# Performance work log

Hardware: AMD Instinct MI355X
Metric: run time of the kernel (lower is better)

## Reference

```python
import jax, jax.numpy as jnp
import numpy as np

B, N, D_IN = 8, 2048, 512
H = 1024          # MLP hidden
D_EMB = 512       # embed output dim
D_ATTN = 256      # attn_layers[-1]; KQ MLP outputs 2*D_ATTN


def setup_inputs() -> dict:
    key = jax.random.key(0)
    ks = jax.random.split(key, 9)
    s = lambda fi, fo: (2.0 / (fi + fo)) ** 0.5
    return {
        "x": jax.random.normal(ks[0], (B, N, D_IN), dtype=jnp.float32),
        # embed MLP: Linear(D_IN,H), ReLU, Linear(H,D_EMB)  (weights stored [in,out])
        "We1": jax.random.normal(ks[1], (D_IN, H), dtype=jnp.float32) * s(D_IN, H),
        "be1": jnp.zeros((H,), dtype=jnp.float32),
        "We2": jax.random.normal(ks[2], (H, D_EMB), dtype=jnp.float32) * s(H, D_EMB),
        "be2": jnp.zeros((D_EMB,), dtype=jnp.float32),
        # KQ MLP: Linear(D_IN,H), ReLU, Linear(H, 2*D_ATTN)
        "Wk1": jax.random.normal(ks[3], (D_IN, H), dtype=jnp.float32) * s(D_IN, H),
        "bk1": jnp.zeros((H,), dtype=jnp.float32),
        "Wk2": jax.random.normal(ks[4], (H, 2 * D_ATTN), dtype=jnp.float32) * s(H, 2 * D_ATTN),
        "bk2": jnp.zeros((2 * D_ATTN,), dtype=jnp.float32),
    }


def reference(x, We1, be1, We2, be2, Wk1, bk1, Wk2, bk2):
    # embed MLP
    embs = jax.nn.relu(x @ We1 + be1) @ We2 + be2            # [B,N,D_EMB]
    # KQ MLP; chunk: first half K, second half Q
    kq = jax.nn.relu(x @ Wk1 + bk1) @ Wk2 + bk2              # [B,N,2*D_ATTN]
    K, Q = kq[..., :D_ATTN], kq[..., D_ATTN:]
    # unscaled attention: softmax(Q K^T) V
    scores = jnp.einsum("bqd,bkd->bqk", Q, K)                # [B,N,N]
    A = jax.nn.softmax(scores, axis=-1)
    return jnp.einsum("bqk,bkd->bqd", A, embs)               # [B,N,D_EMB]
```

## Files before the change

kernel.cpp:

```cpp
#include <hip/hip_runtime.h>
#include <stdint.h>

using fx4   = __attribute__((ext_vector_type(4))) float;
using half8 = __attribute__((ext_vector_type(8))) _Float16;

__device__ __forceinline__ ushort f2h(float x) {
  _Float16 h = (_Float16)x;
  union { _Float16 hv; ushort u; } v; v.hv = h;
  return v.u;
}

__device__ __forceinline__ void gload_lds16(const ushort* g, ushort* l) {
  __builtin_amdgcn_global_load_lds(
      (__attribute__((address_space(1))) const void*)g,
      (__attribute__((address_space(3))) void*)l, 16, 0, 0);
}

#define MFMA16(a, b, c) __builtin_amdgcn_mfma_f32_16x16x32_f16(a, b, c, 0, 0, 0)

__device__ __forceinline__ void gemm_body(
    const ushort* __restrict__ A, int lda,
    const ushort* __restrict__ B, int ldb,
    const float* __restrict__ bias,
    void* __restrict__ C, int ldc,
    int K, int flags, int bx, int by,
    ushort* As, ushort* Bs)
{
  const int tid  = threadIdx.x;
  const int lane = tid & 63;
  const int wave = tid >> 6;
  const int wm   = (wave >> 1) * 64;
  const int wn   = (wave & 1) * 64;
  const long long bm = (long long)by * 128;
  const long long bn = (long long)bx * 128;

  const int srow = tid >> 2;
  const int skq  = (tid & 3) * 8;
  const ushort* a0 = A + (bm + srow) * lda + skq;
  const ushort* a1 = a0 + 64LL * lda;
  const ushort* b0 = B + (bn + srow) * ldb + skq;
  const ushort* b1 = b0 + 64LL * ldb;
  ushort* lA0 = &As[tid * 8];
  ushort* lA1 = &As[2048 + tid * 8];
  ushort* lB0 = &Bs[tid * 8];
  ushort* lB1 = &Bs[2048 + tid * 8];

  fx4 acc[4][4] = {};
  const ushort* ap = &As[(wm + (lane & 15)) * 32 + (lane >> 4) * 8];
  const ushort* bp = &Bs[(wn + (lane & 15)) * 32 + (lane >> 4) * 8];

  for (int k0 = 0; k0 < K; k0 += 32) {
    gload_lds16(a0, lA0);
    gload_lds16(a1, lA1);
    gload_lds16(b0, lB0);
    gload_lds16(b1, lB1);
    a0 += 32; a1 += 32; b0 += 32; b1 += 32;
    __syncthreads();
    half8 af[4], bv[4];
#pragma unroll
    for (int t = 0; t < 4; ++t) {
      af[t] = *(const half8*)(ap + t * 16 * 32);
      bv[t] = *(const half8*)(bp + t * 16 * 32);
    }
#pragma unroll
    for (int i = 0; i < 4; ++i)
#pragma unroll
      for (int j = 0; j < 4; ++j)
        acc[i][j] = MFMA16(af[i], bv[j], acc[i][j]);
    __syncthreads();
  }

  const int col0 = (int)bn + wn + (lane & 15);
  const int row0 = (int)bm + wm + ((lane >> 4) << 2);

  if (flags & 16) {
    ushort* Ch = (ushort*)C;
#pragma unroll
    for (int j = 0; j < 4; ++j) {
      const int col = col0 + j * 16;
      const float bvv = bias ? bias[col] : 0.0f;
#pragma unroll
      for (int i = 0; i < 4; ++i) {
        const int row = row0 + i * 16;
        ushort4 o;
        o.x = f2h(acc[i][j][0] + bvv);
        o.y = f2h(acc[i][j][1] + bvv);
        o.z = f2h(acc[i][j][2] + bvv);
        o.w = f2h(acc[i][j][3] + bvv);
        *(ushort4*)(Ch + (long long)col * ldc + row) = o;
      }
    }
    return;
  }

  float*  Cf = (float*)C;
  ushort* Ch = (ushort*)C;
#pragma unroll
  for (int j = 0; j < 4; ++j) {
    const int col = col0 + j * 16;
    const float bvv = bias ? bias[col] : 0.0f;
#pragma unroll
    for (int i = 0; i < 4; ++i) {
      const long long row = row0 + i * 16;
#pragma unroll
      for (int r = 0; r < 4; ++r) {
        float v = acc[i][j][r] + bvv;
        if (flags & 1) v = fmaxf(v, 0.0f);
        if (flags & 2) Ch[(row + r) * ldc + col] = f2h(v);
        else           Cf[(row + r) * ldc + col] = v;
      }
    }
  }
}

__global__ __launch_bounds__(256)
void gemm_bt(const ushort* __restrict__ A, int lda, long long sA,
             const ushort* __restrict__ B, int ldb, long long sB,
             const float* __restrict__ bias,
             void* __restrict__ C, int ldc, long long sC,
             int K, int flags)
{
  __shared__ ushort As[128 * 32];
  __shared__ ushort Bs[128 * 32];
  const int z = blockIdx.z;
  void* Cz = (flags & (2 | 16)) ? (void*)((ushort*)C + (long long)z * sC)
                                : (void*)((float*)C + (long long)z * sC);
  gemm_body(A + (long long)z * sA, lda, B + (long long)z * sB, ldb, bias,
            Cz, ldc, K, flags, blockIdx.x, blockIdx.y, As, Bs);
}

__global__ __launch_bounds__(256)
void gemm2_pair(const ushort* __restrict__ H, const ushort* __restrict__ W2c,
                const float* __restrict__ be2, const float* __restrict__ bk2,
                ushort* __restrict__ EMBT, ushort* __restrict__ KQ)
{
  __shared__ ushort As[128 * 32];
  __shared__ ushort Bs[128 * 32];
  if (blockIdx.z == 0)
    gemm_body(H, 2048, W2c, 1024, be2, EMBT, 16384, 1024, 16,
              blockIdx.x, blockIdx.y, As, Bs);
  else
    gemm_body(H + 1024, 2048, W2c + 524288, 1024, bk2, KQ, 512, 1024, 2,
              blockIdx.x, blockIdx.y, As, Bs);
}

__global__ __launch_bounds__(512, 2)
void attn_fused(const ushort* __restrict__ KQ, const ushort* __restrict__ EMBT,
                float* __restrict__ out)
{
  __shared__ ushort Qs[20480];
  __shared__ ushort Ps[10240];
  __shared__ float  rmax[256];
  __shared__ float  mstate[64];
  __shared__ float  mnewA[64];
  __shared__ float  alphaA[64];
  __shared__ float  lred[256];

  const int tid  = threadIdx.x;
  const int lane = tid & 63;
  const int w    = tid >> 6;
  const int c    = lane & 15;
  const int q4   = lane >> 4;
  const int qw   = w >> 2;
  const int tw   = w & 3;
  const int dw   = w * 64;
  const int z    = blockIdx.x;
  const long long tb = (long long)z * 2048;
  const int q0   = blockIdx.y * 64;

#pragma unroll
  for (int p = 0; p < 4; ++p) {
    const int cu  = p * 512 + tid;
    const int row = cu >> 5;
    const int kch = cu & 31;
    const int dc  = kch >> 2, qg = kch & 3;
    const half8 v = *(const half8*)(KQ + (tb + q0 + row) * 512 + 256 + dc * 32 + qg * 8);
    *(half8*)(Qs + dc * 2560 + row * 40 + qg * 8) = v;
  }
  if (tid < 64) mstate[tid] = -3.0e38f;
  __syncthreads();

  float l_part[2][4] = {};
  fx4 o[4][4] = {};

  for (int t0 = 0; t0 < 2048; t0 += 128) {
    half8 kb[2][8];
    const ushort* kb0 = KQ + (tb + t0 + tw * 32 + c) * 512;
    const ushort* kb1 = kb0 + 16 * 512;
#pragma unroll
    for (int dc = 0; dc < 8; ++dc) {
      kb[0][dc] = *(const half8*)(kb0 + dc * 32 + q4 * 8);
      kb[1][dc] = *(const half8*)(kb1 + dc * 32 + q4 * 8);
    }
    fx4 s[2][2] = {};
#pragma unroll
    for (int dc = 0; dc < 8; ++dc) {
      const half8 a0 = *(const half8*)(Qs + dc * 2560 + (qw * 32 + c) * 40 + q4 * 8);
      const half8 a1 = *(const half8*)(Qs + dc * 2560 + (qw * 32 + 16 + c) * 40 + q4 * 8);
      s[0][0] = MFMA16(a0, kb[0][dc], s[0][0]); s[0][1] = MFMA16(a0, kb[1][dc], s[0][1]);
      s[1][0] = MFMA16(a1, kb[0][dc], s[1][0]); s[1][1] = MFMA16(a1, kb[1][dc], s[1][1]);
    }
    half8 vb[4][4];
#pragma unroll
    for (int kc = 0; kc < 4; ++kc)
#pragma unroll
      for (int n = 0; n < 4; ++n)
        vb[kc][n] = *(const half8*)(EMBT + (long long)(dw + n * 16 + c) * 16384 +
                                    tb + t0 + kc * 32 + q4 * 8);
#pragma unroll
    for (int i = 0; i < 2; ++i) {
      fx4 rm;
#pragma unroll
      for (int r = 0; r < 4; ++r) rm[r] = fmaxf(s[i][0][r], s[i][1][r]);
#pragma unroll
      for (int off = 1; off < 16; off <<= 1)
#pragma unroll
        for (int r = 0; r < 4; ++r) rm[r] = fmaxf(rm[r], __shfl_xor(rm[r], off, 64));
      if (c == 0) {
#pragma unroll
        for (int r = 0; r < 4; ++r)
          rmax[tw * 64 + qw * 32 + i * 16 + q4 * 4 + r] = rm[r];
      }
    }
    __syncthreads();
    if (w == 0) {
      const float mo = mstate[lane];
      float mn = fmaxf(fmaxf(rmax[lane], rmax[64 + lane]),
                       fmaxf(rmax[128 + lane], rmax[192 + lane]));
      mn = fmaxf(mn, mo);
      mnewA[lane]  = mn;
      alphaA[lane] = __expf(mo - mn);
      mstate[lane] = mn;
    }
    __syncthreads();
#pragma unroll
    for (int i = 0; i < 2; ++i)
#pragma unroll
      for (int r = 0; r < 4; ++r) {
        const int q = qw * 32 + i * 16 + q4 * 4 + r;
        const float mn = mnewA[q];
        const float e0 = __expf(s[i][0][r] - mn);
        const float e1 = __expf(s[i][1][r] - mn);
        l_part[i][r] = alphaA[q] * l_part[i][r] + e0 + e1;
        Ps[tw * 2560 + q * 40 + c]      = f2h(e0);
        Ps[tw * 2560 + q * 40 + 16 + c] = f2h(e1);
      }
#pragma unroll
    for (int i4 = 0; i4 < 4; ++i4)
#pragma unroll
      for (int r = 0; r < 4; ++r) {
        const float aq = alphaA[i4 * 16 + q4 * 4 + r];
#pragma unroll
        for (int n = 0; n < 4; ++n) o[i4][n][r] *= aq;
      }
    __syncthreads();
#pragma unroll
    for (int kc = 0; kc < 4; ++kc) {
      half8 pa[4];
#pragma unroll
      for (int i4 = 0; i4 < 4; ++i4)
        pa[i4] = *(const half8*)(Ps + kc * 2560 + (i4 * 16 + c) * 40 + q4 * 8);
#pragma unroll
      for (int i4 = 0; i4 < 4; ++i4)
#pragma unroll
        for (int n = 0; n < 4; ++n)
          o[i4][n] = MFMA16(pa[i4], vb[kc][n], o[i4][n]);
    }
  }

#pragma unroll
  for (int i = 0; i < 2; ++i) {
    fx4 lv;
#pragma unroll
    for (int r = 0; r < 4; ++r) lv[r] = l_part[i][r];
#pragma unroll
    for (int off = 1; off < 16; off <<= 1)
#pragma unroll
      for (int r = 0; r < 4; ++r) lv[r] += __shfl_xor(lv[r], off, 64);
    if (c == 0) {
#pragma unroll
      for (int r = 0; r < 4; ++r)
        lred[tw * 64 + qw * 32 + i * 16 + q4 * 4 + r] = lv[r];
    }
  }
  __syncthreads();
  if (w == 0)
    alphaA[lane] = 1.0f / (lred[lane] + lred[64 + lane] + lred[128 + lane] + lred[192 + lane]);
  __syncthreads();

  float* ob = out + (tb + q0) * 512 + dw;
#pragma unroll
  for (int i4 = 0; i4 < 4; ++i4)
#pragma unroll
    for (int r = 0; r < 4; ++r) {
      const int q = i4 * 16 + q4 * 4 + r;
      const float li = alphaA[q];
#pragma unroll
      for (int n = 0; n < 4; ++n)
        ob[(long long)q * 512 + n * 16 + c] = o[i4][n][r] * li;
    }
}

__global__ __launch_bounds__(256)
void transpose_cast_w2(const float* __restrict__ in0, const float* __restrict__ in1,
                       ushort* __restrict__ out0, ushort* __restrict__ out1,
                       int R, int C) {
  __shared__ float tile[32][33];
  const float* in  = blockIdx.z ? in1 : in0;
  ushort*      outp = blockIdx.z ? out1 : out0;
  const int c0 = blockIdx.x * 32, r0 = blockIdx.y * 32;
  const int tx = threadIdx.x & 31, ty = threadIdx.x >> 5;
#pragma unroll
  for (int i = 0; i < 32; i += 8)
    tile[ty + i][tx] = in[(long long)(r0 + ty + i) * C + (c0 + tx)];
  __syncthreads();
#pragma unroll
  for (int i = 0; i < 32; i += 8)
    outp[(long long)(c0 + ty + i) * R + (r0 + tx)] = f2h(tile[tx][ty + i]);
}

__global__ __launch_bounds__(256)
void cast_f32_f16(const float* __restrict__ in, ushort* __restrict__ out) {
  const long long i = ((long long)blockIdx.x * 256 + threadIdx.x) * 4;
  const float4 v = *(const float4*)(in + i);
  ushort4 o;
  o.x = f2h(v.x); o.y = f2h(v.y); o.z = f2h(v.z); o.w = f2h(v.w);
  *(ushort4*)(out + i) = o;
}

__global__ __launch_bounds__(256)
void concat_bias(const float* __restrict__ b0, const float* __restrict__ b1,
                 float* __restrict__ out) {
  const int i = blockIdx.x * 256 + threadIdx.x;
  out[i] = (i < 1024) ? b0[i] : b1[i - 1024];
}

extern "C" void kernel_launch(void* const* d_in, const int* in_sizes, int n_in,
                              void* d_out, int out_size, void* d_ws, size_t ws_size,
                              hipStream_t stream) {
  (void)in_sizes; (void)n_in; (void)out_size; (void)ws_size;
  const float* x   = (const float*)d_in[0];
  const float* We1 = (const float*)d_in[1];
  const float* be1 = (const float*)d_in[2];
  const float* We2 = (const float*)d_in[3];
  const float* be2 = (const float*)d_in[4];
  const float* Wk1 = (const float*)d_in[5];
  const float* bk1 = (const float*)d_in[6];
  const float* Wk2 = (const float*)d_in[7];
  const float* bk2 = (const float*)d_in[8];
  float* out = (float*)d_out;
  char* ws = (char*)d_ws;

  ushort* Xb   = (ushort*)(ws + 0);
  ushort* W2c  = (ushort*)(ws + 0);
  ushort* H    = (ushort*)(ws + 16777216);
  ushort* EMBT = (ushort*)(ws + 83886080);
  ushort* KQ   = (ushort*)(ws + 100663296);
  float*  b1c  = (float*)(ws + 117440512);
  ushort* W1c  = (ushort*)(ws + 117448704);

  cast_f32_f16<<<dim3(8192), 256, 0, stream>>>(x, Xb);
  transpose_cast_w2<<<dim3(32, 16, 2), 256, 0, stream>>>(We1, Wk1, W1c, W1c + 524288, 512, 1024);
  concat_bias<<<dim3(8), 256, 0, stream>>>(be1, bk1, b1c);

  gemm_bt<<<dim3(16, 128, 1), 256, 0, stream>>>(Xb, 512, 0, W1c, 512, 0, b1c,
                                                H, 2048, 0, 512, 1 | 2);

  transpose_cast_w2<<<dim3(16, 32, 2), 256, 0, stream>>>(We2, Wk2, W2c, W2c + 524288, 1024, 512);

  gemm2_pair<<<dim3(4, 128, 2), 256, 0, stream>>>(H, W2c, be2, bk2, EMBT, KQ);

  attn_fused<<<dim3(8, 32), 512, 0, stream>>>(KQ, EMBT, out);
}
```

Baseline: 353.9 us.

## Restructure attention kernel with LDS-staged K/V tiles and per-wave softmax state

Rewrites the fused attention kernel to use 256-thread blocks covering 32 queries, loading 32-token K and V tiles into LDS via async global-to-LDS loads. Each wave keeps its own running max and sum in registers, removing the cross-wave max/sum reductions and the extra barriers of the old design. Q fragments are read directly from global each iteration instead of from LDS. The smaller query tile doubles the grid and the total K/V traffic from global, and the short key tiles add more barriers per token, with no double buffering.

```diff
diff --git a/kernel.cpp b/kernel.cpp
--- a/kernel.cpp
+++ b/kernel.cpp
@@ -144,161 +144,105 @@
               blockIdx.x, blockIdx.y, As, Bs);
 }
 
-__global__ __launch_bounds__(512, 2)
+__global__ __launch_bounds__(256, 2)
 void attn_fused(const ushort* __restrict__ KQ, const ushort* __restrict__ EMBT,
                 float* __restrict__ out)
 {
-  __shared__ ushort Qs[20480];
-  __shared__ ushort Ps[10240];
-  __shared__ float  rmax[256];
-  __shared__ float  mstate[64];
-  __shared__ float  mnewA[64];
-  __shared__ float  alphaA[64];
-  __shared__ float  lred[256];
+  __shared__ ushort Ks[8 * 32 * 32];
+  __shared__ ushort Vs[512 * 32];
+  __shared__ ushort Ps[4 * 16 * 40];
 
   const int tid  = threadIdx.x;
   const int lane = tid & 63;
   const int w    = tid >> 6;
   const int c    = lane & 15;
-  const int q4   = lane >> 4;
-  const int qw   = w >> 2;
-  const int tw   = w & 3;
-  const int dw   = w * 64;
+  const int quad = lane >> 4;
+  const int qg   = w & 1;
+  const int dh   = (w >> 1) * 256;
   const int z    = blockIdx.x;
   const long long tb = (long long)z * 2048;
-  const int q0   = blockIdx.y * 64;
-
-#pragma unroll
-  for (int p = 0; p < 4; ++p) {
-    const int cu  = p * 512 + tid;
-    const int row = cu >> 5;
-    const int kch = cu & 31;
-    const int dc  = kch >> 2, qg = kch & 3;
-    const half8 v = *(const half8*)(KQ + (tb + q0 + row) * 512 + 256 + dc * 32 + qg * 8);
-    *(half8*)(Qs + dc * 2560 + row * 40 + qg * 8) = v;
+  const int q0   = blockIdx.y * 32;
+
+  ushort* Pw = Ps + w * 640;
+  const ushort* Qg = KQ + (tb + q0 + qg * 16 + c) * 512 + 256 + quad * 8;
+
+  float m_r[4], l_r[4];
+#pragma unroll
+  for (int r = 0; r < 4; ++r) { m_r[r] = -3.0e38f; l_r[r] = 0.0f; }
+  fx4 o[16] = {};
+
+  for (int t0 = 0; t0 < 2048; t0 += 32) {
+#pragma unroll
+    for (int i = 0; i < 4; ++i) {
+      const int u = i * 256 + tid;
+      const int dc = u >> 7, tok = (u >> 2) & 31, c8 = (u & 3) * 8;
+      gload_lds16(KQ + (tb + t0 + tok) * 512 + dc * 32 + c8, Ks + u * 8);
+    }
+#pragma unroll
+    for (int i = 0; i < 8; ++i) {
+      const int u = i * 256 + tid;
+      const int d = u >> 2, c8 = (u & 3) * 8;
+      gload_lds16(EMBT + (long long)d * 16384 + tb + t0 + c8, Vs + u * 8);
+    }
+    __syncthreads();
+
+    fx4 s[2] = {};
+#pragma unroll
+    for (int dc = 0; dc < 8; ++dc) {
+      const half8 a  = *(const half8*)(Qg + dc * 32);
+      const half8 b0 = *(const half8*)(Ks + dc * 1024 + c * 32 + quad * 8);
+      const half8 b1 = *(const half8*)(Ks + dc * 1024 + (16 + c) * 32 + quad * 8);
+      s[0] = MFMA16(a, b0, s[0]);
+      s[1] = MFMA16(a, b1, s[1]);
+    }
+
+    fx4 rm;
+#pragma unroll
+    for (int r = 0; r < 4; ++r) rm[r] = fmaxf(s[0][r], s[1][r]);
+#pragma unroll
+    for (int off = 1; off < 16; off <<= 1)
+#pragma unroll
+      for (int r = 0; r < 4; ++r) rm[r] = fmaxf(rm[r], __shfl_xor(rm[r], off, 64));
+    float alpha[4];
+#pragma unroll
+    for (int r = 0; r < 4; ++r) {
+      const float mn = fmaxf(m_r[r], rm[r]);
+      alpha[r] = __expf(m_r[r] - mn);
+      m_r[r] = mn;
+      const float e0 = __expf(s[0][r] - mn);
+      const float e1 = __expf(s[1][r] - mn);
+      l_r[r] = alpha[r] * l_r[r] + e0 + e1;
+      Pw[(quad * 4 + r) * 40 + c]      = f2h(e0);
+      Pw[(quad * 4 + r) * 40 + 16 + c] = f2h(e1);
+    }
+#pragma unroll
+    for (int n = 0; n < 16; ++n)
+#pragma unroll
+      for (int r = 0; r < 4; ++r) o[n][r] *= alpha[r];
+
+    const half8 pa = *(const half8*)(Pw + c * 40 + quad * 8);
+#pragma unroll
+    for (int n = 0; n < 16; ++n) {
+      const half8 vb = *(const half8*)(Vs + (dh + n * 16 + c) * 32 + quad * 8);
+      o[n] = MFMA16(pa, vb, o[n]);
+    }
+    __syncthreads();
   }
-  if (tid < 64) mstate[tid] = -3.0e38f;
-  __syncthreads();
-
-  float l_part[2][4] = {};
-  fx4 o[4][4] = {};
-
-  for (int t0 = 0; t0 < 2048; t0 += 128) {
-    half8 kb[2][8];
-    const ushort* kb0 = KQ + (tb + t0 + tw * 32 + c) * 512;
-    const ushort* kb1 = kb0 + 16 * 512;
-#pragma unroll
-    for (int dc = 0; dc < 8; ++dc) {
-      kb[0][dc] = *(const half8*)(kb0 + dc * 32 + q4 * 8);
-      kb[1][dc] = *(const half8*)(kb1 + dc * 32 + q4 * 8);
-    }
-    fx4 s[2][2] = {};
-#pragma unroll
-    for (int dc = 0; dc < 8; ++dc) {
-      const half8 a0 = *(const half8*)(Qs + dc * 2560 + (qw * 32 + c) * 40 + q4 * 8);
-      const half8 a1 = *(const half8*)(Qs + dc * 2560 + (qw * 32 + 16 + c) * 40 + q4 * 8);
-      s[0][0] = MFMA16(a0, kb[0][dc], s[0][0]); s[0][1] = MFMA16(a0, kb[1][dc], s[0][1]);
-      s[1][0] = MFMA16(a1, kb[0][dc], s[1][0]); s[1][1] = MFMA16(a1, kb[1][dc], s[1][1]);
-    }
-    half8 vb[4][4];
-#pragma unroll
-    for (int kc = 0; kc < 4; ++kc)
-#pragma unroll
-      for (int n = 0; n < 4; ++n)
-        vb[kc][n] = *(const half8*)(EMBT + (long long)(dw + n * 16 + c) * 16384 +
-                                    tb + t0 + kc * 32 + q4 * 8);
-#pragma unroll
-    for (int i = 0; i < 2; ++i) {
-      fx4 rm;
-#pragma unroll
-      for (int r = 0; r < 4; ++r) rm[r] = fmaxf(s[i][0][r], s[i][1][r]);
-#pragma unroll
-      for (int off = 1; off < 16; off <<= 1)
-#pragma unroll
-        for (int r = 0; r < 4; ++r) rm[r] = fmaxf(rm[r], __shfl_xor(rm[r], off, 64));
-      if (c == 0) {
-#pragma unroll
-        for (int r = 0; r < 4; ++r)
-          rmax[tw * 64 + qw * 32 + i * 16 + q4 * 4 + r] = rm[r];
-      }
-    }
-    __syncthreads();
-    if (w == 0) {
-      const float mo = mstate[lane];
-      float mn = fmaxf(fmaxf(rmax[lane], rmax[64 + lane]),
-                       fmaxf(rmax[128 + lane], rmax[192 + lane]));
-      mn = fmaxf(mn, mo);
-      mnewA[lane]  = mn;
-      alphaA[lane] = __expf(mo - mn);
-      mstate[lane] = mn;
-    }
-    __syncthreads();
-#pragma unroll
-    for (int i = 0; i < 2; ++i)
-#pragma unroll
-      for (int r = 0; r < 4; ++r) {
-        const int q = qw * 32 + i * 16 + q4 * 4 + r;
-        const float mn = mnewA[q];
-        const float e0 = __expf(s[i][0][r] - mn);
-        const float e1 = __expf(s[i][1][r] - mn);
-        l_part[i][r] = alphaA[q] * l_part[i][r] + e0 + e1;
-        Ps[tw * 2560 + q * 40 + c]      = f2h(e0);
-        Ps[tw * 2560 + q * 40 + 16 + c] = f2h(e1);
-      }
-#pragma unroll
-    for (int i4 = 0; i4 < 4; ++i4)
-#pragma unroll
-      for (int r = 0; r < 4; ++r) {
-        const float aq = alphaA[i4 * 16 + q4 * 4 + r];
-#pragma unroll
-        for (int n = 0; n < 4; ++n) o[i4][n][r] *= aq;
-      }
-    __syncthreads();
-#pragma unroll
-    for (int kc = 0; kc < 4; ++kc) {
-      half8 pa[4];
-#pragma unroll
-      for (int i4 = 0; i4 < 4; ++i4)
-        pa[i4] = *(const half8*)(Ps + kc * 2560 + (i4 * 16 + c) * 40 + q4 * 8);
-#pragma unroll
-      for (int i4 = 0; i4 < 4; ++i4)
-#pragma unroll
-        for (int n = 0; n < 4; ++n)
-          o[i4][n] = MFMA16(pa[i4], vb[kc][n], o[i4][n]);
-    }
-  }
-
-#pragma unroll
-  for (int i = 0; i < 2; ++i) {
-    fx4 lv;
-#pragma unroll
-    for (int r = 0; r < 4; ++r) lv[r] = l_part[i][r];
-#pragma unroll
-    for (int off = 1; off < 16; off <<= 1)
-#pragma unroll
-      for (int r = 0; r < 4; ++r) lv[r] += __shfl_xor(lv[r], off, 64);
-    if (c == 0) {
-#pragma unroll
-      for (int r = 0; r < 4; ++r)
-        lred[tw * 64 + qw * 32 + i * 16 + q4 * 4 + r] = lv[r];
-    }
-  }
-  __syncthreads();
-  if (w == 0)
-    alphaA[lane] = 1.0f / (lred[lane] + lred[64 + lane] + lred[128 + lane] + lred[192 + lane]);
-  __syncthreads();
-
-  float* ob = out + (tb + q0) * 512 + dw;
-#pragma unroll
-  for (int i4 = 0; i4 < 4; ++i4)
-#pragma unroll
-    for (int r = 0; r < 4; ++r) {
-      const int q = i4 * 16 + q4 * 4 + r;
-      const float li = alphaA[q];
-#pragma unroll
-      for (int n = 0; n < 4; ++n)
-        ob[(long long)q * 512 + n * 16 + c] = o[i4][n][r] * li;
-    }
+
+#pragma unroll
+  for (int off = 1; off < 16; off <<= 1)
+#pragma unroll
+    for (int r = 0; r < 4; ++r) l_r[r] += __shfl_xor(l_r[r], off, 64);
+  float linv[4];
+#pragma unroll
+  for (int r = 0; r < 4; ++r) linv[r] = 1.0f / l_r[r];
+
+  float* ob = out + (tb + q0 + qg * 16) * 512 + dh;
+#pragma unroll
+  for (int n = 0; n < 16; ++n)
+#pragma unroll
+    for (int r = 0; r < 4; ++r)
+      ob[(long long)(quad * 4 + r) * 512 + n * 16 + c] = o[n][r] * linv[r];
 }
 
 __global__ __launch_bounds__(256)
@@ -370,5 +314,5 @@
 
   gemm2_pair<<<dim3(4, 128, 2), 256, 0, stream>>>(H, W2c, be2, bk2, EMBT, KQ);
 
-  attn_fused<<<dim3(8, 32), 512, 0, stream>>>(KQ, EMBT, out);
-}
+  attn_fused<<<dim3(8, 64), 256, 0, stream>>>(KQ, EMBT, out);
+}
```

Result: slower. 490.0 us (+38.4%).

## Store K and V in 32-token tiled layouts for contiguous attention loads

Applied to the files above, without the earlier changes.

The second-layer GEMM epilogue now writes K into 32x32 tiles per token block and V^T into per-32-token panels, and writes Q to its own dense buffer. The attention kernel reads K and V from these tiles, so each 128-token step touches a few contiguous 2-16 KB chunks instead of rows strided across a 512-wide or 16384-wide matrix. The goal is better coalescing and cache locality for the K/V loads in the inner loop. In exchange, the K epilogue now does scattered scalar 16-bit stores with a branch per element, which may make the GEMM epilogue slower.

```diff
diff --git a/kernel.cpp b/kernel.cpp
--- a/kernel.cpp
+++ b/kernel.cpp
@@ -24,7 +24,7 @@
     const float* __restrict__ bias,
     void* __restrict__ C, int ldc,
     int K, int flags, int bx, int by,
-    ushort* As, ushort* Bs)
+    ushort* As, ushort* Bs, ushort* __restrict__ C2 = nullptr)
 {
   const int tid  = threadIdx.x;
   const int lane = tid & 63;
@@ -87,7 +87,32 @@
         o.y = f2h(acc[i][j][1] + bvv);
         o.z = f2h(acc[i][j][2] + bvv);
         o.w = f2h(acc[i][j][3] + bvv);
-        *(ushort4*)(Ch + (long long)col * ldc + row) = o;
+        *(ushort4*)(Ch + (long long)(row >> 5) * 16384 + (long long)col * 32 + (row & 31)) = o;
+      }
+    }
+    return;
+  }
+
+  if (flags & 32) {
+    ushort* KTp = (ushort*)C;
+#pragma unroll
+    for (int j = 0; j < 4; ++j) {
+      const int col = col0 + j * 16;
+      const float bvv = bias ? bias[col] : 0.0f;
+#pragma unroll
+      for (int i = 0; i < 4; ++i) {
+        const int row = row0 + i * 16;
+#pragma unroll
+        for (int r = 0; r < 4; ++r) {
+          const float v = acc[i][j][r] + bvv;
+          if (col < 256) {
+            const int tok = row + r;
+            KTp[(long long)(tok >> 5) * 8192 + (col >> 5) * 1024 +
+                (tok & 31) * 32 + (col & 31)] = f2h(v);
+          } else {
+            C2[(long long)(row + r) * 256 + (col - 256)] = f2h(v);
+          }
+        }
       }
     }
     return;
@@ -123,8 +148,8 @@
   __shared__ ushort As[128 * 32];
   __shared__ ushort Bs[128 * 32];
   const int z = blockIdx.z;
-  void* Cz = (flags & (2 | 16)) ? (void*)((ushort*)C + (long long)z * sC)
-                                : (void*)((float*)C + (long long)z * sC);
+  void* Cz = (flags & 2) ? (void*)((ushort*)C + (long long)z * sC)
+                         : (void*)((float*)C + (long long)z * sC);
   gemm_body(A + (long long)z * sA, lda, B + (long long)z * sB, ldb, bias,
             Cz, ldc, K, flags, blockIdx.x, blockIdx.y, As, Bs);
 }
@@ -132,21 +157,22 @@
 __global__ __launch_bounds__(256)
 void gemm2_pair(const ushort* __restrict__ H, const ushort* __restrict__ W2c,
                 const float* __restrict__ be2, const float* __restrict__ bk2,
-                ushort* __restrict__ EMBT, ushort* __restrict__ KQ)
+                ushort* __restrict__ VT, ushort* __restrict__ KT,
+                ushort* __restrict__ Qm)
 {
   __shared__ ushort As[128 * 32];
   __shared__ ushort Bs[128 * 32];
   if (blockIdx.z == 0)
-    gemm_body(H, 2048, W2c, 1024, be2, EMBT, 16384, 1024, 16,
+    gemm_body(H, 2048, W2c, 1024, be2, VT, 0, 1024, 16,
               blockIdx.x, blockIdx.y, As, Bs);
   else
-    gemm_body(H + 1024, 2048, W2c + 524288, 1024, bk2, KQ, 512, 1024, 2,
-              blockIdx.x, blockIdx.y, As, Bs);
+    gemm_body(H + 1024, 2048, W2c + 524288, 1024, bk2, KT, 0, 1024, 32,
+              blockIdx.x, blockIdx.y, As, Bs, Qm);
 }
 
 __global__ __launch_bounds__(512, 2)
-void attn_fused(const ushort* __restrict__ KQ, const ushort* __restrict__ EMBT,
-                float* __restrict__ out)
+void attn_fused(const ushort* __restrict__ KT, const ushort* __restrict__ VT,
+                const ushort* __restrict__ Qm, float* __restrict__ out)
 {
   __shared__ ushort Qs[20480];
   __shared__ ushort Ps[10240];
@@ -166,6 +192,7 @@
   const int dw   = w * 64;
   const int z    = blockIdx.x;
   const long long tb = (long long)z * 2048;
+  const long long pbase = (long long)z * 64;
   const int q0   = blockIdx.y * 64;
 
 #pragma unroll
@@ -174,7 +201,7 @@
     const int row = cu >> 5;
     const int kch = cu & 31;
     const int dc  = kch >> 2, qg = kch & 3;
-    const half8 v = *(const half8*)(KQ + (tb + q0 + row) * 512 + 256 + dc * 32 + qg * 8);
+    const half8 v = *(const half8*)(Qm + (tb + q0 + row) * 256 + dc * 32 + qg * 8);
     *(half8*)(Qs + dc * 2560 + row * 40 + qg * 8) = v;
   }
   if (tid < 64) mstate[tid] = -3.0e38f;
@@ -184,13 +211,13 @@
   fx4 o[4][4] = {};
 
   for (int t0 = 0; t0 < 2048; t0 += 128) {
+    const long long pt = pbase + (t0 >> 5);
     half8 kb[2][8];
-    const ushort* kb0 = KQ + (tb + t0 + tw * 32 + c) * 512;
-    const ushort* kb1 = kb0 + 16 * 512;
+    const ushort* kp = KT + (pt + tw) * 8192;
 #pragma unroll
     for (int dc = 0; dc < 8; ++dc) {
-      kb[0][dc] = *(const half8*)(kb0 + dc * 32 + q4 * 8);
-      kb[1][dc] = *(const half8*)(kb1 + dc * 32 + q4 * 8);
+      kb[0][dc] = *(const half8*)(kp + dc * 1024 + c * 32 + q4 * 8);
+      kb[1][dc] = *(const half8*)(kp + dc * 1024 + (16 + c) * 32 + q4 * 8);
     }
     fx4 s[2][2] = {};
 #pragma unroll
@@ -205,8 +232,8 @@
     for (int kc = 0; kc < 4; ++kc)
 #pragma unroll
       for (int n = 0; n < 4; ++n)
-        vb[kc][n] = *(const half8*)(EMBT + (long long)(dw + n * 16 + c) * 16384 +
-                                    tb + t0 + kc * 32 + q4 * 8);
+        vb[kc][n] = *(const half8*)(VT + (pt + kc) * 16384 +
+                                    (dw + n * 16 + c) * 32 + q4 * 8);
 #pragma unroll
     for (int i = 0; i < 2; ++i) {
       fx4 rm;
@@ -351,13 +378,14 @@
   float* out = (float*)d_out;
   char* ws = (char*)d_ws;
 
-  ushort* Xb   = (ushort*)(ws + 0);
-  ushort* W2c  = (ushort*)(ws + 0);
-  ushort* H    = (ushort*)(ws + 16777216);
-  ushort* EMBT = (ushort*)(ws + 83886080);
-  ushort* KQ   = (ushort*)(ws + 100663296);
-  float*  b1c  = (float*)(ws + 117440512);
-  ushort* W1c  = (ushort*)(ws + 117448704);
+  ushort* Xb  = (ushort*)(ws + 0);
+  ushort* W2c = (ushort*)(ws + 0);
+  ushort* H   = (ushort*)(ws + 16777216);
+  ushort* VT  = (ushort*)(ws + 83886080);
+  ushort* KT  = (ushort*)(ws + 100663296);
+  ushort* Qm  = (ushort*)(ws + 109051904);
+  float*  b1c = (float*)(ws + 117440512);
+  ushort* W1c = (ushort*)(ws + 117448704);
 
   cast_f32_f16<<<dim3(8192), 256, 0, stream>>>(x, Xb);
   transpose_cast_w2<<<dim3(32, 16, 2), 256, 0, stream>>>(We1, Wk1, W1c, W1c + 524288, 512, 1024);
@@ -368,7 +396,7 @@
 
   transpose_cast_w2<<<dim3(16, 32, 2), 256, 0, stream>>>(We2, Wk2, W2c, W2c + 524288, 1024, 512);
 
-  gemm2_pair<<<dim3(4, 128, 2), 256, 0, stream>>>(H, W2c, be2, bk2, EMBT, KQ);
-
-  attn_fused<<<dim3(8, 32), 512, 0, stream>>>(KQ, EMBT, out);
-}
+  gemm2_pair<<<dim3(4, 128, 2), 256, 0, stream>>>(H, W2c, be2, bk2, VT, KT, Qm);
+
+  attn_fused<<<dim3(8, 32), 512, 0, stream>>>(KT, VT, Qm, out);
+}
```

Measured after the change: 314.8 us. -11.1%, faster.
